# Optimization experiments

Measured on AMD Instinct MI355X. Metric: run time of the kernel, lower is better.

The kernel has to match this reference:

```python
import jax, jax.numpy as jnp
import numpy as np

B, T, D, E, P = 32, 8192, 256, 16, 64  # batch, tokens, dim, num_spectral_blocks, pixels_per_patch


def setup_inputs() -> dict:
    key = jax.random.key(0)
    k1, k2, k3, k4 = jax.random.split(key, 4)
    x = jax.random.normal(k1, (B, T, D), dtype=jnp.float32)
    block_indices = jax.random.randint(k2, (B, T), 0, E)
    # per-expert Linear(dim -> pixels_per_patch): weight [E, D, P], bias [E, P]
    W = jax.random.normal(k3, (E, D, P), dtype=jnp.float32) * 0.02
    b = jax.random.normal(k4, (E, P), dtype=jnp.float32) * 0.02
    return {"x": x, "W": W, "b": b, "block_indices": block_indices}


def reference(x, W, b, block_indices):
    # Each token [b, t] is routed to expert block_indices[b, t]; that expert's
    # Linear(dim -> pixels_per_patch) produces the output row. Loop is over the
    # small fixed expert count (16), fully vectorized over tokens.
    num_experts = W.shape[0]
    out = jnp.zeros(x.shape[:2] + (W.shape[2],), dtype=x.dtype)
    for e in range(num_experts):
        y = x @ W[e] + b[e]                       # [B, T, P]
        sel = (block_indices == e)[..., None]      # [B, T, 1]
        out = jnp.where(sel, y, out)
    return out
```

## Files before the change

kernel.cpp:

```cpp
#include <hip/hip_runtime.h>

#define NT (32 * 8192)
#define DIM 256
#define NE 16
#define NP 64
#define MT 32


typedef short bf16x8 __attribute__((ext_vector_type(8)));
typedef float f32x4 __attribute__((ext_vector_type(4)));

__device__ __forceinline__ unsigned short f2bf(float f) {
  unsigned int u = __builtin_bit_cast(unsigned int, f);
  u += 0x7fffu + ((u >> 16) & 1u);
  return (unsigned short)(u >> 16);
}

__global__ void k_hist(const int* __restrict__ idx, int* __restrict__ partials) {
  __shared__ int h[NE];
  int t = threadIdx.x;
  if (t < NE) h[t] = 0;
  __syncthreads();
  int base = blockIdx.x * 4096;
  #pragma unroll
  for (int i = 0; i < 16; ++i) {
    int e = idx[base + i * 256 + t];
    atomicAdd(&h[e], 1);
  }
  __syncthreads();
  if (t < NE) partials[blockIdx.x * NE + t] = h[t];
}

__global__ void k_scan(const int* __restrict__ partials, int* __restrict__ offsets,
                       int* __restrict__ base_be) {
  __shared__ int totals[NE];
  __shared__ int eoff[NE + 1];
  int t = threadIdx.x;
  if (t < NE) {
    int run = 0;
    for (int b = 0; b < 64; ++b) {
      base_be[b * NE + t] = run;
      run += partials[b * NE + t];
    }
    totals[t] = run;
  }
  __syncthreads();
  if (t == 0) {
    int run = 0;
    for (int e = 0; e < NE; ++e) { eoff[e] = run; run += totals[e]; }
    eoff[NE] = run;
    for (int e = 0; e <= NE; ++e) offsets[e] = eoff[e];
  }
  __syncthreads();
  if (t < NE) {
    int eo = eoff[t];
    for (int b = 0; b < 64; ++b) base_be[b * NE + t] += eo;
  }
}

__global__ void k_scatter(const int* __restrict__ idx, const int* __restrict__ base_be,
                          int* __restrict__ bucket) {
  __shared__ int lbase[NE];
  __shared__ int lcur[NE];
  int t = threadIdx.x;
  if (t < NE) { lbase[t] = base_be[blockIdx.x * NE + t]; lcur[t] = 0; }
  __syncthreads();
  int base = blockIdx.x * 4096;
  #pragma unroll
  for (int i = 0; i < 16; ++i) {
    int tok = base + i * 256 + t;
    int e = idx[tok];
    int pos = atomicAdd(&lcur[e], 1);
    bucket[lbase[e] + pos] = tok;
  }
}

__global__ void k_wconv(const float* __restrict__ W, unsigned short* __restrict__ Wt) {
  int gid = blockIdx.x * 256 + threadIdx.x;
  int e = gid >> 10;
  int n = (gid >> 4) & 63;
  int k0 = (gid & 15) << 4;
  const float* src = W + e * (DIM * NP) + n;
  unsigned short* dst = Wt + ((e * NP + n) * DIM + k0);
  #pragma unroll
  for (int j = 0; j < 16; ++j) dst[j] = f2bf(src[(k0 + j) * NP]);
}

__global__ __launch_bounds__(256) void k_gemm(
    const float* __restrict__ x, const unsigned short* __restrict__ Wt,
    const float* __restrict__ bvec, const int* __restrict__ offsets,
    const int* __restrict__ bucket, float* __restrict__ out) {
  __shared__ unsigned short xt[MT][DIM + 8];
  __shared__ int tok[MT];

  int tid = blockIdx.x;
  int e = -1, row0 = 0, rows = 0;
  #pragma unroll 1
  for (int ee = 0; ee < NE; ++ee) {
    int beg = offsets[ee];
    int c = offsets[ee + 1] - beg;
    int ntile = (c + MT - 1) >> 5;
    if (tid < ntile) {
      e = ee;
      row0 = beg + (tid << 5);
      rows = c - (tid << 5);
      if (rows > MT) rows = MT;
      break;
    }
    tid -= ntile;
  }
  if (e < 0) return;

  int t = threadIdx.x;
  int w = t >> 6;
  int lane = t & 63;
  int cc = lane & 15, q = lane >> 4;
  int m_base = (w & 1) << 4;
  int nf_base = (w >> 1) << 1;

  const unsigned short* wb = Wt + (e * NP) * DIM;
  bf16x8 bfr[2][8];
  #pragma unroll
  for (int i = 0; i < 2; ++i) {
    int n = (nf_base + i) * 16 + cc;
    #pragma unroll
    for (int ks = 0; ks < 8; ++ks)
      bfr[i][ks] = *(const bf16x8*)(wb + n * DIM + ks * 32 + q * 8);
  }
  float bias[2];
  #pragma unroll
  for (int i = 0; i < 2; ++i) bias[i] = bvec[e * NP + (nf_base + i) * 16 + cc];

  if (t < MT) tok[t] = bucket[row0 + (t < rows ? t : 0)];
  __syncthreads();

  {
    int r = t >> 3, s = t & 7;
    const float* xr = x + (long)tok[r] * DIM;
    unsigned short* dst = &xt[r][0];
    #pragma unroll
    for (int j = 0; j < 8; ++j) {
      float4 v = *(const float4*)(xr + s * 4 + j * 32);
      ushort4 pk = make_ushort4(f2bf(v.x), f2bf(v.y), f2bf(v.z), f2bf(v.w));
      *(ushort4*)(dst + s * 4 + j * 32) = pk;
    }
  }
  __syncthreads();

  f32x4 acc0 = {0.f, 0.f, 0.f, 0.f};
  f32x4 acc1 = {0.f, 0.f, 0.f, 0.f};
  const unsigned short* arow = &xt[m_base + cc][0];
  #pragma unroll
  for (int ks = 0; ks < 8; ++ks) {
    bf16x8 a = *(const bf16x8*)(arow + ks * 32 + q * 8);
    acc0 = __builtin_amdgcn_mfma_f32_16x16x32_bf16(a, bfr[0][ks], acc0, 0, 0, 0);
    acc1 = __builtin_amdgcn_mfma_f32_16x16x32_bf16(a, bfr[1][ks], acc1, 0, 0, 0);
  }

  #pragma unroll
  for (int i = 0; i < 2; ++i) {
    int col = (nf_base + i) * 16 + cc;
    #pragma unroll
    for (int r = 0; r < 4; ++r) {
      int m = m_base + q * 4 + r;
      if (m < rows) {
        float v = (i == 0 ? acc0[r] : acc1[r]) + bias[i];
        out[(long)tok[m] * NP + col] = v;
      }
    }
  }
}

extern "C" void kernel_launch(void* const* d_in, const int* in_sizes, int n_in,
                              void* d_out, int out_size, void* d_ws, size_t ws_size,
                              hipStream_t stream) {
  const float* x = (const float*)d_in[0];
  const float* W = (const float*)d_in[1];
  const float* b = (const float*)d_in[2];
  const int* idx = (const int*)d_in[3];
  float* out = (float*)d_out;

  int* ws = (int*)d_ws;
  int* offsets = ws;
  int* base_be = ws + 32;
  int* partials = ws + 2048;
  int* bucket = ws + 4096;
  unsigned short* Wt = (unsigned short*)(ws + 4096 + NT);

  k_hist<<<64, 256, 0, stream>>>(idx, partials);
  k_wconv<<<64, 256, 0, stream>>>(W, Wt);
  k_scan<<<1, 64, 0, stream>>>(partials, offsets, base_be);
  k_scatter<<<64, 256, 0, stream>>>(idx, base_be, bucket);
  k_gemm<<<(NT / MT) + NE, 256, 0, stream>>>(x, Wt, b, offsets, bucket, out);
}
```

Before: 433.9 us.

## Make GEMM blocks persistent per expert, looping over token tiles

The grouped GEMM now launches a fixed grid of 16 experts times 64 slices. Each block loads its expert's weight fragments into registers once and then loops over that expert's token tiles with a stride of 64. This drops the per-tile weight reload and the serial expert search each block did before. Each block now processes tiles one after another with no overlap between loading and computing, so parallelism per block drops and load balance depends on the expert counts.

After: 429.8 us. Within noise of the previous version (-0.9%).

```diff
diff --git a/kernel.cpp b/kernel.cpp
--- a/kernel.cpp
+++ b/kernel.cpp
@@ -5,7 +5,7 @@
 #define NE 16
 #define NP 64
 #define MT 32
-
+#define NSLICE 64
 
 typedef short bf16x8 __attribute__((ext_vector_type(8)));
 typedef float f32x4 __attribute__((ext_vector_type(4)));
@@ -91,25 +91,12 @@
     const float* __restrict__ bvec, const int* __restrict__ offsets,
     const int* __restrict__ bucket, float* __restrict__ out) {
   __shared__ unsigned short xt[MT][DIM + 8];
-  __shared__ int tok[MT];
 
-  int tid = blockIdx.x;
-  int e = -1, row0 = 0, rows = 0;
-  #pragma unroll 1
-  for (int ee = 0; ee < NE; ++ee) {
-    int beg = offsets[ee];
-    int c = offsets[ee + 1] - beg;
-    int ntile = (c + MT - 1) >> 5;
-    if (tid < ntile) {
-      e = ee;
-      row0 = beg + (tid << 5);
-      rows = c - (tid << 5);
-      if (rows > MT) rows = MT;
-      break;
-    }
-    tid -= ntile;
-  }
-  if (e < 0) return;
+  int e = blockIdx.x >> 6;
+  int slice = blockIdx.x & (NSLICE - 1);
+  int beg = offsets[e];
+  int cnt = offsets[e + 1] - beg;
+  int ntiles = (cnt + MT - 1) >> 5;
 
   int t = threadIdx.x;
   int w = t >> 6;
@@ -131,41 +118,47 @@
   #pragma unroll
   for (int i = 0; i < 2; ++i) bias[i] = bvec[e * NP + (nf_base + i) * 16 + cc];
 
-  if (t < MT) tok[t] = bucket[row0 + (t < rows ? t : 0)];
-  __syncthreads();
+  int sr = t >> 3, ss = t & 7;
 
-  {
-    int r = t >> 3, s = t & 7;
-    const float* xr = x + (long)tok[r] * DIM;
-    unsigned short* dst = &xt[r][0];
+  for (int it = slice; it < ntiles; it += NSLICE) {
+    int row0 = beg + (it << 5);
+    int rows = cnt - (it << 5);
+    if (rows > MT) rows = MT;
+
+    __syncthreads();
+
+    {
+      int rr = sr < rows ? sr : 0;
+      int tokr = bucket[row0 + rr];
+      const float* xr = x + (long)tokr * DIM;
+      unsigned short* dst = &xt[sr][0];
+      #pragma unroll
+      for (int j = 0; j < 8; ++j) {
+        float4 v = *(const float4*)(xr + ss * 4 + j * 32);
+        ushort4 pk = make_ushort4(f2bf(v.x), f2bf(v.y), f2bf(v.z), f2bf(v.w));
+        *(ushort4*)(dst + ss * 4 + j * 32) = pk;
+      }
+    }
+    __syncthreads();
+
+    f32x4 acc0 = {0.f, 0.f, 0.f, 0.f};
+    f32x4 acc1 = {0.f, 0.f, 0.f, 0.f};
+    const unsigned short* arow = &xt[m_base + cc][0];
     #pragma unroll
-    for (int j = 0; j < 8; ++j) {
-      float4 v = *(const float4*)(xr + s * 4 + j * 32);
-      ushort4 pk = make_ushort4(f2bf(v.x), f2bf(v.y), f2bf(v.z), f2bf(v.w));
-      *(ushort4*)(dst + s * 4 + j * 32) = pk;
+    for (int ks = 0; ks < 8; ++ks) {
+      bf16x8 a = *(const bf16x8*)(arow + ks * 32 + q * 8);
+      acc0 = __builtin_amdgcn_mfma_f32_16x16x32_bf16(a, bfr[0][ks], acc0, 0, 0, 0);
+      acc1 = __builtin_amdgcn_mfma_f32_16x16x32_bf16(a, bfr[1][ks], acc1, 0, 0, 0);
     }
-  }
-  __syncthreads();
 
-  f32x4 acc0 = {0.f, 0.f, 0.f, 0.f};
-  f32x4 acc1 = {0.f, 0.f, 0.f, 0.f};
-  const unsigned short* arow = &xt[m_base + cc][0];
-  #pragma unroll
-  for (int ks = 0; ks < 8; ++ks) {
-    bf16x8 a = *(const bf16x8*)(arow + ks * 32 + q * 8);
-    acc0 = __builtin_amdgcn_mfma_f32_16x16x32_bf16(a, bfr[0][ks], acc0, 0, 0, 0);
-    acc1 = __builtin_amdgcn_mfma_f32_16x16x32_bf16(a, bfr[1][ks], acc1, 0, 0, 0);
-  }
-
-  #pragma unroll
-  for (int i = 0; i < 2; ++i) {
-    int col = (nf_base + i) * 16 + cc;
     #pragma unroll
     for (int r = 0; r < 4; ++r) {
       int m = m_base + q * 4 + r;
       if (m < rows) {
-        float v = (i == 0 ? acc0[r] : acc1[r]) + bias[i];
-        out[(long)tok[m] * NP + col] = v;
+        int tk = bucket[row0 + m];
+        float* orow = out + (long)tk * NP + cc;
+        orow[nf_base * 16] = acc0[r] + bias[0];
+        orow[(nf_base + 1) * 16] = acc1[r] + bias[1];
       }
     }
   }
@@ -191,5 +184,5 @@
   k_wconv<<<64, 256, 0, stream>>>(W, Wt);
   k_scan<<<1, 64, 0, stream>>>(partials, offsets, base_be);
   k_scatter<<<64, 256, 0, stream>>>(idx, base_be, bucket);
-  k_gemm<<<(NT / MT) + NE, 256, 0, stream>>>(x, Wt, b, offsets, bucket, out);
+  k_gemm<<<NE * NSLICE, 256, 0, stream>>>(x, Wt, b, offsets, bucket, out);
 }
```
